# Optimization experiments

Hardware: AMD Instinct MI355X
Metric: run time of the kernel (lower is better)

Reference implementation:

```python
import jax, jax.numpy as jnp
import numpy as np

N = 100000   # nodes
E = 1600000  # edges (avg degree 16)
DIN, DH, DOUT = 128, 64, 40


def setup_inputs() -> dict:
    key = jax.random.key(0)
    ks = jax.random.split(key, 6)
    x = jax.random.normal(ks[0], (N, DIN), dtype=jnp.float32)
    edge_index = jax.random.randint(ks[1], (2, E), 0, N, dtype=jnp.int32)
    s1 = float(1.0 / np.sqrt(DIN))
    s2 = float(1.0 / np.sqrt(DH))
    W1 = jax.random.uniform(ks[2], (DIN, DH), jnp.float32, -s1, s1)
    b1 = jax.random.uniform(ks[3], (DH,), jnp.float32, -s1, s1)
    W2 = jax.random.uniform(ks[4], (DH, DOUT), jnp.float32, -s2, s2)
    b2 = jax.random.uniform(ks[5], (DOUT,), jnp.float32, -s2, s2)
    return {"x": x, "W1": W1, "b1": b1, "W2": W2, "b2": b2, "edge_index": edge_index}


def _gcn_conv(x, W, b, src, dst):
    """PyG GCNConv: add self-loops, symmetric degree normalization, scatter-add."""
    n = x.shape[0]
    h = x @ W  # [N, F_out] — transform before propagation (PyG order)
    ones = jnp.ones(src.shape[0], dtype=h.dtype)
    deg = jax.ops.segment_sum(ones, dst, num_segments=n) + 1.0  # +1 for self-loop
    dinv = jax.lax.rsqrt(deg)  # deg >= 1, no zero guard needed
    norm = dinv[src] * dinv[dst]  # [E]
    agg = jax.ops.segment_sum(h[src] * norm[:, None], dst, num_segments=n)
    agg = agg + h * (dinv * dinv)[:, None]  # self-loop messages
    return agg + b


def reference(x, W1, b1, W2, b2, edge_index):
    src, dst = edge_index[0], edge_index[1]
    h = jax.nn.relu(_gcn_conv(x, W1, b1, src, dst))
    out = _gcn_conv(h, W2, b2, src, dst)
    return jax.nn.log_softmax(out, axis=1)
```

## Files before the change

kernel.cpp:

```cpp
#include <hip/hip_runtime.h>
#include <hip/hip_fp16.h>
#include <math.h>

#define N_NODES 100000
#define N_EDGES 1600000
#define DIN 128
#define DH 64
#define DOUT 40

#define NB 256
#define BN 391
#define CAP 8192
#define BIN_BLOCKS 256
#define EPB 6250

typedef unsigned short u16;
typedef unsigned int u32;

__device__ inline __half2 u2h(u32 u) {
    union { u32 x; __half2 h; } c; c.x = u; return c.h;
}
__device__ inline u32 h2u(__half2 h) {
    union { __half2 h; u32 x; } c; c.h = h; return c.x;
}


__global__ __launch_bounds__(256) void k_bin(const int* __restrict__ src,
                                             const int* __restrict__ dst,
                                             int* __restrict__ gcur,
                                             u32* __restrict__ staged) {
    __shared__ int hist[NB];
    __shared__ int base[NB];
    __shared__ int cur[NB];
    int t = threadIdx.x;
    for (int i = t; i < NB; i += 256) { hist[i] = 0; cur[i] = 0; }
    __syncthreads();
    int e0 = blockIdx.x * EPB;
    int e1 = e0 + EPB; if (e1 > N_EDGES) e1 = N_EDGES;
    for (int e = e0 + t; e < e1; e += 256)
        atomicAdd(&hist[dst[e] / BN], 1);
    __syncthreads();
    for (int i = t; i < NB; i += 256) {
        int h = hist[i];
        base[i] = h ? atomicAdd(&gcur[i], h) : 0;
    }
    __syncthreads();
    for (int e = e0 + t; e < e1; e += 256) {
        int d = dst[e], s = src[e];
        int b = d / BN;
        int dl = d - b * BN;
        int r = base[b] + atomicAdd(&cur[b], 1);
        if (r < CAP) staged[(size_t)b * CAP + r] = (u32)s | ((u32)dl << 17);
    }
}


__global__ __launch_bounds__(256) void k_csr(const int* __restrict__ gcur,
                                             const u32* __restrict__ staged,
                                             int* __restrict__ csr,
                                             int4* __restrict__ meta,
                                             float* __restrict__ dinv) {
    __shared__ u32 sedge[CAP];
    __shared__ int lcsr[CAP];
    __shared__ int hist[BN];
    __shared__ int lrs[BN];
    __shared__ int cur[BN];
    __shared__ int sbuf[256];
    int b = blockIdx.x, t = threadIdx.x;

    int part = 0;
    for (int i = t; i < b; i += 256) {
        int c = gcur[i]; if (c > CAP) c = CAP;
        part += c;
    }
    sbuf[t] = part;
    __syncthreads();
    for (int off = 128; off; off >>= 1) {
        if (t < off) sbuf[t] += sbuf[t + off];
        __syncthreads();
    }
    int base_ = sbuf[0];
    __syncthreads();

    int cnt = gcur[b]; if (cnt > CAP) cnt = CAP;
    for (int i = t; i < BN; i += 256) hist[i] = 0;
    for (int i = t; i < cnt; i += 256) sedge[i] = staged[(size_t)b * CAP + i];
    __syncthreads();
    for (int i = t; i < cnt; i += 256) atomicAdd(&hist[sedge[i] >> 17], 1);
    __syncthreads();

    int v0 = (2 * t < BN) ? hist[2 * t] : 0;
    int v1 = (2 * t + 1 < BN) ? hist[2 * t + 1] : 0;
    int s = v0 + v1;
    sbuf[t] = s;
    __syncthreads();
    for (int off = 1; off < 256; off <<= 1) {
        int add = (t >= off) ? sbuf[t - off] : 0;
        __syncthreads();
        sbuf[t] += add;
        __syncthreads();
    }
    int excl = sbuf[t] - s;
    if (2 * t < BN)     { lrs[2 * t] = excl;      cur[2 * t] = excl; }
    if (2 * t + 1 < BN) { lrs[2 * t + 1] = excl + v0; cur[2 * t + 1] = excl + v0; }
    __syncthreads();

    for (int i = t; i < cnt; i += 256) {
        u32 p = sedge[i];
        int pos = atomicAdd(&cur[p >> 17], 1);
        lcsr[pos] = (int)((p & 0x1FFFF) << 3);
    }
    __syncthreads();

    for (int i = t; i < cnt; i += 256) csr[base_ + i] = lcsr[i];
    int n0 = b * BN;
    for (int i = t; i < BN; i += 256) {
        int n = n0 + i;
        if (n < N_NODES) {
            int dg = hist[i];
            float dv = rsqrtf((float)dg + 1.0f);
            meta[n] = make_int4(base_ + lrs[i], dg, __float_as_int(dv), 0);
            dinv[n] = dv;
        }
    }
}


__global__ __launch_bounds__(256) void k_gemm1(const float* __restrict__ x,
                                               const float* __restrict__ W1,
                                               const float* __restrict__ dinv,
                                               u16* __restrict__ h1s) {
    __shared__ float xs[64 * 140];
    __shared__ float wsh[DIN * DH];
    int t = threadIdx.x;
    int row0 = blockIdx.x * 64;

    for (int it = 0; it < 8; ++it) {
        int idx = (it * 256 + t) * 4;
        int r = idx >> 7, c = idx & 127;
        float4 v = make_float4(0.f, 0.f, 0.f, 0.f);
        if (row0 + r < N_NODES) v = *(const float4*)&x[(size_t)(row0 + r) * DIN + c];
        *(float4*)&xs[r * 140 + c] = v;
    }
    for (int it = 0; it < 8; ++it) {
        int idx = (it * 256 + t) * 4;
        *(float4*)&wsh[idx] = *(const float4*)&W1[idx];
    }
    __syncthreads();

    int tr = t & 15;
    int tc = t >> 4;
    float acc[4][4] = {};
    for (int kb = 0; kb < DIN; kb += 4) {
        float4 w0 = *(const float4*)&wsh[(kb + 0) * DH + tr * 4];
        float4 w1 = *(const float4*)&wsh[(kb + 1) * DH + tr * 4];
        float4 w2 = *(const float4*)&wsh[(kb + 2) * DH + tr * 4];
        float4 w3 = *(const float4*)&wsh[(kb + 3) * DH + tr * 4];
#pragma unroll
        for (int i = 0; i < 4; ++i) {
            float4 xv = *(const float4*)&xs[(tc * 4 + i) * 140 + kb];
            acc[i][0] += xv.x * w0.x; acc[i][1] += xv.x * w0.y;
            acc[i][2] += xv.x * w0.z; acc[i][3] += xv.x * w0.w;
            acc[i][0] += xv.y * w1.x; acc[i][1] += xv.y * w1.y;
            acc[i][2] += xv.y * w1.z; acc[i][3] += xv.y * w1.w;
            acc[i][0] += xv.z * w2.x; acc[i][1] += xv.z * w2.y;
            acc[i][2] += xv.z * w2.z; acc[i][3] += xv.z * w2.w;
            acc[i][0] += xv.w * w3.x; acc[i][1] += xv.w * w3.y;
            acc[i][2] += xv.w * w3.z; acc[i][3] += xv.w * w3.w;
        }
    }
#pragma unroll
    for (int i = 0; i < 4; ++i) {
        int row = row0 + tc * 4 + i;
        if (row < N_NODES) {
            float dv = dinv[row];
            ushort4 o;
            o.x = __half_as_ushort(__float2half(acc[i][0] * dv));
            o.y = __half_as_ushort(__float2half(acc[i][1] * dv));
            o.z = __half_as_ushort(__float2half(acc[i][2] * dv));
            o.w = __half_as_ushort(__float2half(acc[i][3] * dv));
            *(ushort4*)&h1s[(size_t)row * DH + tr * 4] = o;
        }
    }
}


__global__ __launch_bounds__(256) void k_agg1(const u16* __restrict__ h1s,
                                              const int4* __restrict__ meta,
                                              const int* __restrict__ csr,
                                              const float* __restrict__ b1,
                                              float* __restrict__ h1) {
    int node = blockIdx.x * 4 + (threadIdx.x >> 6);
    if (node >= N_NODES) return;
    node = __builtin_amdgcn_readfirstlane(node);
    int lane = threadIdx.x & 63;
    int es = lane >> 3, fq = lane & 7;
    int4 me = meta[node];
    int s0 = me.x, d = me.y;
    float dv = __int_as_float(me.z);
    const uint4* rows = (const uint4*)h1s;
    __half2 A0 = __float2half2_rn(0.f), A1 = A0, A2 = A0, A3 = A0;
    if (es == 0) {
        uint4 v = rows[(u32)(node * 8 + fq)];
        A0 = u2h(v.x); A1 = u2h(v.y); A2 = u2h(v.z); A3 = u2h(v.w);
    }
    for (int base = 0; base < d; base += 64) {
        int nn = d - base; if (nn > 64) nn = 64;
        int myidx = (lane < nn) ? csr[s0 + base + lane] : 0;
        int j = 0;
        for (; j + 16 <= nn; j += 16) {
            int x0 = __builtin_amdgcn_ds_bpermute((j + es) * 4, myidx);
            int x1 = __builtin_amdgcn_ds_bpermute((j + 8 + es) * 4, myidx);
            uint4 v0 = rows[(u32)(x0 + fq)];
            uint4 v1 = rows[(u32)(x1 + fq)];
            A0 = __hadd2(A0, u2h(v0.x)); A1 = __hadd2(A1, u2h(v0.y));
            A2 = __hadd2(A2, u2h(v0.z)); A3 = __hadd2(A3, u2h(v0.w));
            A0 = __hadd2(A0, u2h(v1.x)); A1 = __hadd2(A1, u2h(v1.y));
            A2 = __hadd2(A2, u2h(v1.z)); A3 = __hadd2(A3, u2h(v1.w));
        }
        for (; j < nn; j += 8) {
            int x = __builtin_amdgcn_ds_bpermute((j + es) * 4, myidx);
            if (j + es < nn) {
                uint4 v = rows[(u32)(x + fq)];
                A0 = __hadd2(A0, u2h(v.x)); A1 = __hadd2(A1, u2h(v.y));
                A2 = __hadd2(A2, u2h(v.z)); A3 = __hadd2(A3, u2h(v.w));
            }
        }
    }
#pragma unroll
    for (int off = 8; off <= 32; off <<= 1) {
        A0 = __hadd2(A0, u2h((u32)__shfl_xor((int)h2u(A0), off, 64)));
        A1 = __hadd2(A1, u2h((u32)__shfl_xor((int)h2u(A1), off, 64)));
        A2 = __hadd2(A2, u2h((u32)__shfl_xor((int)h2u(A2), off, 64)));
        A3 = __hadd2(A3, u2h((u32)__shfl_xor((int)h2u(A3), off, 64)));
    }
    if (es == 0) {
        float4 bva = ((const float4*)b1)[fq * 2 + 0];
        float4 bvb = ((const float4*)b1)[fq * 2 + 1];
        float4 oa, ob;
        oa.x = fmaxf(__low2float(A0)  * dv + bva.x, 0.f);
        oa.y = fmaxf(__high2float(A0) * dv + bva.y, 0.f);
        oa.z = fmaxf(__low2float(A1)  * dv + bva.z, 0.f);
        oa.w = fmaxf(__high2float(A1) * dv + bva.w, 0.f);
        ob.x = fmaxf(__low2float(A2)  * dv + bvb.x, 0.f);
        ob.y = fmaxf(__high2float(A2) * dv + bvb.y, 0.f);
        ob.z = fmaxf(__low2float(A3)  * dv + bvb.z, 0.f);
        ob.w = fmaxf(__high2float(A3) * dv + bvb.w, 0.f);
        ((float4*)h1)[(u32)(node * 16 + fq * 2 + 0)] = oa;
        ((float4*)h1)[(u32)(node * 16 + fq * 2 + 1)] = ob;
    }
}


__global__ __launch_bounds__(256) void k_gemm2(const float* __restrict__ h1,
                                               const float* __restrict__ W2,
                                               const float* __restrict__ dinv,
                                               u16* __restrict__ h2s) {
    __shared__ float xs[64 * 68];
    __shared__ float wsh[DH * DOUT];
    int t = threadIdx.x;
    int row0 = blockIdx.x * 64;

    for (int it = 0; it < 4; ++it) {
        int idx = (it * 256 + t) * 4;
        int r = idx >> 6, c = idx & 63;
        float4 v = make_float4(0.f, 0.f, 0.f, 0.f);
        if (row0 + r < N_NODES) v = *(const float4*)&h1[(size_t)(row0 + r) * DH + c];
        *(float4*)&xs[r * 68 + c] = v;
    }
    for (int idx = t * 4; idx < DH * DOUT; idx += 1024) {
        *(float4*)&wsh[idx] = *(const float4*)&W2[idx];
    }
    __syncthreads();

    int fg = t & 7;
    int rg = t >> 3;
    float acc[2][5] = {};
    for (int k = 0; k < DH; ++k) {
        float x0 = xs[(rg * 2 + 0) * 68 + k];
        float x1 = xs[(rg * 2 + 1) * 68 + k];
#pragma unroll
        for (int j = 0; j < 5; ++j) {
            float w = wsh[k * DOUT + fg * 5 + j];
            acc[0][j] += x0 * w;
            acc[1][j] += x1 * w;
        }
    }
#pragma unroll
    for (int i = 0; i < 2; ++i) {
        int row = row0 + rg * 2 + i;
        if (row < N_NODES) {
            float dvv = dinv[row];
#pragma unroll
            for (int j = 0; j < 5; ++j)
                h2s[(size_t)row * 64 + fg * 5 + j] =
                    __half_as_ushort(__float2half(acc[i][j] * dvv));
        }
    }
}


__global__ __launch_bounds__(256) void k_agg2(const u16* __restrict__ h2s,
                                              const int4* __restrict__ meta,
                                              const int* __restrict__ csr,
                                              const float* __restrict__ b2,
                                              float* __restrict__ out) {
    int node = blockIdx.x * 4 + (threadIdx.x >> 6);
    if (node >= N_NODES) return;
    node = __builtin_amdgcn_readfirstlane(node);
    int lane = threadIdx.x & 63;
    int es = lane >> 3, fq = lane & 7;
    bool act = fq < 5;
    int4 me = meta[node];
    int s0 = me.x, d = me.y;
    float dv = __int_as_float(me.z);
    const uint4* rows = (const uint4*)h2s;
    __half2 A0 = __float2half2_rn(0.f), A1 = A0, A2 = A0, A3 = A0;
    if (es == 0 && act) {
        uint4 v = rows[(u32)(node * 8 + fq)];
        A0 = u2h(v.x); A1 = u2h(v.y); A2 = u2h(v.z); A3 = u2h(v.w);
    }
    for (int base = 0; base < d; base += 64) {
        int nn = d - base; if (nn > 64) nn = 64;
        int myidx = (lane < nn) ? csr[s0 + base + lane] : 0;
        int j = 0;
        for (; j + 16 <= nn; j += 16) {
            int x0 = __builtin_amdgcn_ds_bpermute((j + es) * 4, myidx);
            int x1 = __builtin_amdgcn_ds_bpermute((j + 8 + es) * 4, myidx);
            if (act) {
                uint4 v0 = rows[(u32)(x0 + fq)];
                uint4 v1 = rows[(u32)(x1 + fq)];
                A0 = __hadd2(A0, u2h(v0.x)); A1 = __hadd2(A1, u2h(v0.y));
                A2 = __hadd2(A2, u2h(v0.z)); A3 = __hadd2(A3, u2h(v0.w));
                A0 = __hadd2(A0, u2h(v1.x)); A1 = __hadd2(A1, u2h(v1.y));
                A2 = __hadd2(A2, u2h(v1.z)); A3 = __hadd2(A3, u2h(v1.w));
            }
        }
        for (; j < nn; j += 8) {
            int x = __builtin_amdgcn_ds_bpermute((j + es) * 4, myidx);
            if (act && j + es < nn) {
                uint4 v = rows[(u32)(x + fq)];
                A0 = __hadd2(A0, u2h(v.x)); A1 = __hadd2(A1, u2h(v.y));
                A2 = __hadd2(A2, u2h(v.z)); A3 = __hadd2(A3, u2h(v.w));
            }
        }
    }
#pragma unroll
    for (int off = 8; off <= 32; off <<= 1) {
        A0 = __hadd2(A0, u2h((u32)__shfl_xor((int)h2u(A0), off, 64)));
        A1 = __hadd2(A1, u2h((u32)__shfl_xor((int)h2u(A1), off, 64)));
        A2 = __hadd2(A2, u2h((u32)__shfl_xor((int)h2u(A2), off, 64)));
        A3 = __hadd2(A3, u2h((u32)__shfl_xor((int)h2u(A3), off, 64)));
    }

    float4 bva = act ? ((const float4*)b2)[fq * 2 + 0] : make_float4(0.f, 0.f, 0.f, 0.f);
    float4 bvb = act ? ((const float4*)b2)[fq * 2 + 1] : make_float4(0.f, 0.f, 0.f, 0.f);
    float v0 = act ? __low2float(A0)  * dv + bva.x : -INFINITY;
    float v1 = act ? __high2float(A0) * dv + bva.y : -INFINITY;
    float v2 = act ? __low2float(A1)  * dv + bva.z : -INFINITY;
    float v3 = act ? __high2float(A1) * dv + bva.w : -INFINITY;
    float v4 = act ? __low2float(A2)  * dv + bvb.x : -INFINITY;
    float v5 = act ? __high2float(A2) * dv + bvb.y : -INFINITY;
    float v6 = act ? __low2float(A3)  * dv + bvb.z : -INFINITY;
    float v7 = act ? __high2float(A3) * dv + bvb.w : -INFINITY;
    float m = fmaxf(fmaxf(fmaxf(v0, v1), fmaxf(v2, v3)),
                    fmaxf(fmaxf(v4, v5), fmaxf(v6, v7)));
    m = fmaxf(m, __shfl_xor(m, 1, 64));
    m = fmaxf(m, __shfl_xor(m, 2, 64));
    m = fmaxf(m, __shfl_xor(m, 4, 64));
    float ex = 0.f;
    if (act) {
        ex = __expf(v0 - m) + __expf(v1 - m) + __expf(v2 - m) + __expf(v3 - m)
           + __expf(v4 - m) + __expf(v5 - m) + __expf(v6 - m) + __expf(v7 - m);
    }
    ex += __shfl_xor(ex, 1, 64);
    ex += __shfl_xor(ex, 2, 64);
    ex += __shfl_xor(ex, 4, 64);
    float lse = m + __logf(ex);
    if (es == 0 && act) {
        float4 oa = make_float4(v0 - lse, v1 - lse, v2 - lse, v3 - lse);
        float4 ob = make_float4(v4 - lse, v5 - lse, v6 - lse, v7 - lse);
        *(float4*)&out[(u32)(node * 40 + fq * 8 + 0)] = oa;
        *(float4*)&out[(u32)(node * 40 + fq * 8 + 4)] = ob;
    }
}


extern "C" void kernel_launch(void* const* d_in, const int* in_sizes, int n_in,
                              void* d_out, int out_size, void* d_ws, size_t ws_size,
                              hipStream_t stream) {
    const float* x  = (const float*)d_in[0];
    const float* W1 = (const float*)d_in[1];
    const float* b1 = (const float*)d_in[2];
    const float* W2 = (const float*)d_in[3];
    const float* b2 = (const float*)d_in[4];
    const int* eidx = (const int*)d_in[5];
    const int* srcp = eidx;
    const int* dstp = eidx + N_EDGES;
    float* out = (float*)d_out;

    char* w = (char*)d_ws;
    int* gcur    = (int*)w;   w += sizeof(int) * NB;
    float* dinv  = (float*)w; w += sizeof(float) * N_NODES + 48;
    int4* meta   = (int4*)w;  w += sizeof(int4) * N_NODES;
    u32* staged  = (u32*)w;   w += sizeof(u32) * (size_t)NB * CAP;
    int* csr     = (int*)w;   w += sizeof(int) * N_EDGES;
    u16* h1s     = (u16*)w;   w += sizeof(u16) * (size_t)N_NODES * DH;
    float* h1    = (float*)w; w += sizeof(float) * (size_t)N_NODES * DH;
    u16* h2s     = h1s;

    hipMemsetAsync(gcur, 0, sizeof(int) * NB, stream);
    k_bin<<<BIN_BLOCKS, 256, 0, stream>>>(srcp, dstp, gcur, staged);
    k_csr<<<NB, 256, 0, stream>>>(gcur, staged, csr, meta, dinv);
    k_gemm1<<<(N_NODES + 63) / 64, 256, 0, stream>>>(x, W1, dinv, h1s);
    k_agg1<<<(N_NODES + 3) / 4, 256, 0, stream>>>(h1s, meta, csr, b1, h1);
    k_gemm2<<<(N_NODES + 63) / 64, 256, 0, stream>>>(h1, W2, dinv, h2s);
    k_agg2<<<(N_NODES + 3) / 4, 256, 0, stream>>>(h2s, meta, csr, b2, out);
}
```

Baseline: 213.3 us.

## Merge CSR build and first GEMM into one launch; add nontemporal stores

Computes per-node degree with global atomics during binning, so the first GEMM no longer needs dinv from the CSR kernel. This lets CSR construction and GEMM1 run as disjoint block ranges of a single kernel, overlapping the two and removing one launch. Streaming loads and stores are also marked nontemporal to reduce cache pollution. The cost is 1.6M extra global atomics in the bin kernel, a larger memset, and higher shared-memory use per block, which may lower occupancy for the GEMM blocks.

After: 280.2 us. 1.31x slower.

```diff
diff --git a/kernel.cpp b/kernel.cpp
--- a/kernel.cpp
+++ b/kernel.cpp
@@ -13,21 +13,29 @@
 #define CAP 8192
 #define BIN_BLOCKS 256
 #define EPB 6250
+#define GEMM1_BLOCKS ((N_NODES + 63) / 64)
 
 typedef unsigned short u16;
 typedef unsigned int u32;
+typedef float f32x4 __attribute__((ext_vector_type(4)));
+typedef unsigned short u16x4 __attribute__((ext_vector_type(4)));
 
 __device__ inline __half2 u2h(u32 u) {
     union { u32 x; __half2 h; } c; c.x = u; return c.h;
 }
 __device__ inline u32 h2u(__half2 h) {
     union { __half2 h; u32 x; } c; c.h = h; return c.x;
+}
+__device__ inline void nt_store4(float* p, float a, float b, float c, float d) {
+    f32x4 t = {a, b, c, d};
+    __builtin_nontemporal_store(t, (f32x4*)p);
 }
 
 
 __global__ __launch_bounds__(256) void k_bin(const int* __restrict__ src,
                                              const int* __restrict__ dst,
                                              int* __restrict__ gcur,
+                                             int* __restrict__ deg,
                                              u32* __restrict__ staged) {
     __shared__ int hist[NB];
     __shared__ int base[NB];
@@ -37,8 +45,11 @@
     __syncthreads();
     int e0 = blockIdx.x * EPB;
     int e1 = e0 + EPB; if (e1 > N_EDGES) e1 = N_EDGES;
-    for (int e = e0 + t; e < e1; e += 256)
-        atomicAdd(&hist[dst[e] / BN], 1);
+    for (int e = e0 + t; e < e1; e += 256) {
+        int dd = dst[e];
+        atomicAdd(&hist[dd / BN], 1);
+        atomicAdd(&deg[dd], 1);
+    }
     __syncthreads();
     for (int i = t; i < NB; i += 256) {
         int h = hist[i];
@@ -50,136 +61,143 @@
         int b = d / BN;
         int dl = d - b * BN;
         int r = base[b] + atomicAdd(&cur[b], 1);
-        if (r < CAP) staged[(size_t)b * CAP + r] = (u32)s | ((u32)dl << 17);
-    }
-}
-
-
-__global__ __launch_bounds__(256) void k_csr(const int* __restrict__ gcur,
+        if (r < CAP)
+            __builtin_nontemporal_store((u32)s | ((u32)dl << 17),
+                                        &staged[(size_t)b * CAP + r]);
+    }
+}
+
+
+__global__ __launch_bounds__(256) void k_mid(const int* __restrict__ gcur,
                                              const u32* __restrict__ staged,
                                              int* __restrict__ csr,
                                              int4* __restrict__ meta,
-                                             float* __restrict__ dinv) {
-    __shared__ u32 sedge[CAP];
-    __shared__ int lcsr[CAP];
-    __shared__ int hist[BN];
-    __shared__ int lrs[BN];
-    __shared__ int cur[BN];
-    __shared__ int sbuf[256];
-    int b = blockIdx.x, t = threadIdx.x;
-
-    int part = 0;
-    for (int i = t; i < b; i += 256) {
-        int c = gcur[i]; if (c > CAP) c = CAP;
-        part += c;
-    }
-    sbuf[t] = part;
-    __syncthreads();
-    for (int off = 128; off; off >>= 1) {
-        if (t < off) sbuf[t] += sbuf[t + off];
-        __syncthreads();
-    }
-    int base_ = sbuf[0];
-    __syncthreads();
-
-    int cnt = gcur[b]; if (cnt > CAP) cnt = CAP;
-    for (int i = t; i < BN; i += 256) hist[i] = 0;
-    for (int i = t; i < cnt; i += 256) sedge[i] = staged[(size_t)b * CAP + i];
-    __syncthreads();
-    for (int i = t; i < cnt; i += 256) atomicAdd(&hist[sedge[i] >> 17], 1);
-    __syncthreads();
-
-    int v0 = (2 * t < BN) ? hist[2 * t] : 0;
-    int v1 = (2 * t + 1 < BN) ? hist[2 * t + 1] : 0;
-    int s = v0 + v1;
-    sbuf[t] = s;
-    __syncthreads();
-    for (int off = 1; off < 256; off <<= 1) {
-        int add = (t >= off) ? sbuf[t - off] : 0;
-        __syncthreads();
-        sbuf[t] += add;
-        __syncthreads();
-    }
-    int excl = sbuf[t] - s;
-    if (2 * t < BN)     { lrs[2 * t] = excl;      cur[2 * t] = excl; }
-    if (2 * t + 1 < BN) { lrs[2 * t + 1] = excl + v0; cur[2 * t + 1] = excl + v0; }
-    __syncthreads();
-
-    for (int i = t; i < cnt; i += 256) {
-        u32 p = sedge[i];
-        int pos = atomicAdd(&cur[p >> 17], 1);
-        lcsr[pos] = (int)((p & 0x1FFFF) << 3);
-    }
-    __syncthreads();
-
-    for (int i = t; i < cnt; i += 256) csr[base_ + i] = lcsr[i];
-    int n0 = b * BN;
-    for (int i = t; i < BN; i += 256) {
-        int n = n0 + i;
-        if (n < N_NODES) {
-            int dg = hist[i];
-            float dv = rsqrtf((float)dg + 1.0f);
-            meta[n] = make_int4(base_ + lrs[i], dg, __float_as_int(dv), 0);
-            dinv[n] = dv;
-        }
-    }
-}
-
-
-__global__ __launch_bounds__(256) void k_gemm1(const float* __restrict__ x,
-                                               const float* __restrict__ W1,
-                                               const float* __restrict__ dinv,
-                                               u16* __restrict__ h1s) {
-    __shared__ float xs[64 * 140];
-    __shared__ float wsh[DIN * DH];
+                                             float* __restrict__ dinv,
+                                             const int* __restrict__ deg,
+                                             const float* __restrict__ x,
+                                             const float* __restrict__ W1,
+                                             u16* __restrict__ h1s) {
+    __shared__ __align__(16) char smem[71296];
     int t = threadIdx.x;
-    int row0 = blockIdx.x * 64;
-
-    for (int it = 0; it < 8; ++it) {
-        int idx = (it * 256 + t) * 4;
-        int r = idx >> 7, c = idx & 127;
-        float4 v = make_float4(0.f, 0.f, 0.f, 0.f);
-        if (row0 + r < N_NODES) v = *(const float4*)&x[(size_t)(row0 + r) * DIN + c];
-        *(float4*)&xs[r * 140 + c] = v;
-    }
-    for (int it = 0; it < 8; ++it) {
-        int idx = (it * 256 + t) * 4;
-        *(float4*)&wsh[idx] = *(const float4*)&W1[idx];
-    }
-    __syncthreads();
-
-    int tr = t & 15;
-    int tc = t >> 4;
-    float acc[4][4] = {};
-    for (int kb = 0; kb < DIN; kb += 4) {
-        float4 w0 = *(const float4*)&wsh[(kb + 0) * DH + tr * 4];
-        float4 w1 = *(const float4*)&wsh[(kb + 1) * DH + tr * 4];
-        float4 w2 = *(const float4*)&wsh[(kb + 2) * DH + tr * 4];
-        float4 w3 = *(const float4*)&wsh[(kb + 3) * DH + tr * 4];
+    int blk = blockIdx.x;
+
+    if (blk < NB) {
+        u32* sedge = (u32*)smem;
+        int* lcsr  = (int*)(smem + 32768);
+        int* hist  = (int*)(smem + 65536);
+        int* lrs   = (int*)(smem + 67100);
+        int* cur   = (int*)(smem + 68664);
+        int* sbuf  = (int*)(smem + 70228);
+        int b = blk;
+
+        int part = 0;
+        for (int i = t; i < b; i += 256) {
+            int c = gcur[i]; if (c > CAP) c = CAP;
+            part += c;
+        }
+        sbuf[t] = part;
+        __syncthreads();
+        for (int off = 128; off; off >>= 1) {
+            if (t < off) sbuf[t] += sbuf[t + off];
+            __syncthreads();
+        }
+        int base_ = sbuf[0];
+        __syncthreads();
+
+        int cnt = gcur[b]; if (cnt > CAP) cnt = CAP;
+        for (int i = t; i < BN; i += 256) hist[i] = 0;
+        for (int i = t; i < cnt; i += 256)
+            sedge[i] = __builtin_nontemporal_load(&staged[(size_t)b * CAP + i]);
+        __syncthreads();
+        for (int i = t; i < cnt; i += 256) atomicAdd(&hist[sedge[i] >> 17], 1);
+        __syncthreads();
+
+        int v0 = (2 * t < BN) ? hist[2 * t] : 0;
+        int v1 = (2 * t + 1 < BN) ? hist[2 * t + 1] : 0;
+        int s = v0 + v1;
+        sbuf[t] = s;
+        __syncthreads();
+        for (int off = 1; off < 256; off <<= 1) {
+            int add = (t >= off) ? sbuf[t - off] : 0;
+            __syncthreads();
+            sbuf[t] += add;
+            __syncthreads();
+        }
+        int excl = sbuf[t] - s;
+        if (2 * t < BN)     { lrs[2 * t] = excl;          cur[2 * t] = excl; }
+        if (2 * t + 1 < BN) { lrs[2 * t + 1] = excl + v0; cur[2 * t + 1] = excl + v0; }
+        __syncthreads();
+
+        for (int i = t; i < cnt; i += 256) {
+            u32 p = sedge[i];
+            int pos = atomicAdd(&cur[p >> 17], 1);
+            lcsr[pos] = (int)((p & 0x1FFFF) << 3);
+        }
+        __syncthreads();
+
+        for (int i = t; i < cnt; i += 256)
+            __builtin_nontemporal_store(lcsr[i], &csr[base_ + i]);
+        int n0 = b * BN;
+        for (int i = t; i < BN; i += 256) {
+            int n = n0 + i;
+            if (n < N_NODES) {
+                int dg = hist[i];
+                float dv = rsqrtf((float)dg + 1.0f);
+                meta[n] = make_int4(base_ + lrs[i], dg, __float_as_int(dv), 0);
+                dinv[n] = dv;
+            }
+        }
+    } else {
+        float* xs  = (float*)smem;
+        float* wsh = (float*)(smem + 35840);
+        int row0 = (blk - NB) * 64;
+
+        for (int it = 0; it < 8; ++it) {
+            int idx = (it * 256 + t) * 4;
+            int r = idx >> 7, c = idx & 127;
+            float4 v = make_float4(0.f, 0.f, 0.f, 0.f);
+            if (row0 + r < N_NODES) v = *(const float4*)&x[(size_t)(row0 + r) * DIN + c];
+            *(float4*)&xs[r * 140 + c] = v;
+        }
+        for (int it = 0; it < 8; ++it) {
+            int idx = (it * 256 + t) * 4;
+            *(float4*)&wsh[idx] = *(const float4*)&W1[idx];
+        }
+        __syncthreads();
+
+        int tr = t & 15;
+        int tc = t >> 4;
+        float acc[4][4] = {};
+        for (int kb = 0; kb < DIN; kb += 4) {
+            float4 w0 = *(const float4*)&wsh[(kb + 0) * DH + tr * 4];
+            float4 w1 = *(const float4*)&wsh[(kb + 1) * DH + tr * 4];
+            float4 w2 = *(const float4*)&wsh[(kb + 2) * DH + tr * 4];
+            float4 w3 = *(const float4*)&wsh[(kb + 3) * DH + tr * 4];
+#pragma unroll
+            for (int i = 0; i < 4; ++i) {
+                float4 xv = *(const float4*)&xs[(tc * 4 + i) * 140 + kb];
+                acc[i][0] += xv.x * w0.x; acc[i][1] += xv.x * w0.y;
+                acc[i][2] += xv.x * w0.z; acc[i][3] += xv.x * w0.w;
+                acc[i][0] += xv.y * w1.x; acc[i][1] += xv.y * w1.y;
+                acc[i][2] += xv.y * w1.z; acc[i][3] += xv.y * w1.w;
+                acc[i][0] += xv.z * w2.x; acc[i][1] += xv.z * w2.y;
+                acc[i][2] += xv.z * w2.z; acc[i][3] += xv.z * w2.w;
+                acc[i][0] += xv.w * w3.x; acc[i][1] += xv.w * w3.y;
+                acc[i][2] += xv.w * w3.z; acc[i][3] += xv.w * w3.w;
+            }
+        }
 #pragma unroll
         for (int i = 0; i < 4; ++i) {
-            float4 xv = *(const float4*)&xs[(tc * 4 + i) * 140 + kb];
-            acc[i][0] += xv.x * w0.x; acc[i][1] += xv.x * w0.y;
-            acc[i][2] += xv.x * w0.z; acc[i][3] += xv.x * w0.w;
-            acc[i][0] += xv.y * w1.x; acc[i][1] += xv.y * w1.y;
-            acc[i][2] += xv.y * w1.z; acc[i][3] += xv.y * w1.w;
-            acc[i][0] += xv.z * w2.x; acc[i][1] += xv.z * w2.y;
-            acc[i][2] += xv.z * w2.z; acc[i][3] += xv.z * w2.w;
-            acc[i][0] += xv.w * w3.x; acc[i][1] += xv.w * w3.y;
-            acc[i][2] += xv.w * w3.z; acc[i][3] += xv.w * w3.w;
-        }
-    }
-#pragma unroll
-    for (int i = 0; i < 4; ++i) {
-        int row = row0 + tc * 4 + i;
-        if (row < N_NODES) {
-            float dv = dinv[row];
-            ushort4 o;
-            o.x = __half_as_ushort(__float2half(acc[i][0] * dv));
-            o.y = __half_as_ushort(__float2half(acc[i][1] * dv));
-            o.z = __half_as_ushort(__float2half(acc[i][2] * dv));
-            o.w = __half_as_ushort(__float2half(acc[i][3] * dv));
-            *(ushort4*)&h1s[(size_t)row * DH + tr * 4] = o;
+            int row = row0 + tc * 4 + i;
+            if (row < N_NODES) {
+                float dv = rsqrtf((float)deg[row] + 1.0f);
+                u16x4 o;
+                o.x = __half_as_ushort(__float2half(acc[i][0] * dv));
+                o.y = __half_as_ushort(__float2half(acc[i][1] * dv));
+                o.z = __half_as_ushort(__float2half(acc[i][2] * dv));
+                o.w = __half_as_ushort(__float2half(acc[i][3] * dv));
+                __builtin_nontemporal_store(o, (u16x4*)&h1s[(size_t)row * DH + tr * 4]);
+            }
         }
     }
 }
@@ -206,7 +224,7 @@
     }
     for (int base = 0; base < d; base += 64) {
         int nn = d - base; if (nn > 64) nn = 64;
-        int myidx = (lane < nn) ? csr[s0 + base + lane] : 0;
+        int myidx = (lane < nn) ? __builtin_nontemporal_load(&csr[s0 + base + lane]) : 0;
         int j = 0;
         for (; j + 16 <= nn; j += 16) {
             int x0 = __builtin_amdgcn_ds_bpermute((j + es) * 4, myidx);
@@ -237,17 +255,17 @@
     if (es == 0) {
         float4 bva = ((const float4*)b1)[fq * 2 + 0];
         float4 bvb = ((const float4*)b1)[fq * 2 + 1];
-        float4 oa, ob;
-        oa.x = fmaxf(__low2float(A0)  * dv + bva.x, 0.f);
-        oa.y = fmaxf(__high2float(A0) * dv + bva.y, 0.f);
-        oa.z = fmaxf(__low2float(A1)  * dv + bva.z, 0.f);
-        oa.w = fmaxf(__high2float(A1) * dv + bva.w, 0.f);
-        ob.x = fmaxf(__low2float(A2)  * dv + bvb.x, 0.f);
-        ob.y = fmaxf(__high2float(A2) * dv + bvb.y, 0.f);
-        ob.z = fmaxf(__low2float(A3)  * dv + bvb.z, 0.f);
-        ob.w = fmaxf(__high2float(A3) * dv + bvb.w, 0.f);
-        ((float4*)h1)[(u32)(node * 16 + fq * 2 + 0)] = oa;
-        ((float4*)h1)[(u32)(node * 16 + fq * 2 + 1)] = ob;
+        float* dst0 = &h1[(u32)(node * 64 + fq * 8)];
+        nt_store4(dst0,
+                  fmaxf(__low2float(A0)  * dv + bva.x, 0.f),
+                  fmaxf(__high2float(A0) * dv + bva.y, 0.f),
+                  fmaxf(__low2float(A1)  * dv + bva.z, 0.f),
+                  fmaxf(__high2float(A1) * dv + bva.w, 0.f));
+        nt_store4(dst0 + 4,
+                  fmaxf(__low2float(A2)  * dv + bvb.x, 0.f),
+                  fmaxf(__high2float(A2) * dv + bvb.y, 0.f),
+                  fmaxf(__low2float(A3)  * dv + bvb.z, 0.f),
+                  fmaxf(__high2float(A3) * dv + bvb.w, 0.f));
     }
 }
 
@@ -293,8 +311,9 @@
             float dvv = dinv[row];
 #pragma unroll
             for (int j = 0; j < 5; ++j)
-                h2s[(size_t)row * 64 + fg * 5 + j] =
-                    __half_as_ushort(__float2half(acc[i][j] * dvv));
+                __builtin_nontemporal_store(
+                    (u16)__half_as_ushort(__float2half(acc[i][j] * dvv)),
+                    &h2s[(size_t)row * 64 + fg * 5 + j]);
         }
     }
 }
@@ -322,7 +341,7 @@
     }
     for (int base = 0; base < d; base += 64) {
         int nn = d - base; if (nn > 64) nn = 64;
-        int myidx = (lane < nn) ? csr[s0 + base + lane] : 0;
+        int myidx = (lane < nn) ? __builtin_nontemporal_load(&csr[s0 + base + lane]) : 0;
         int j = 0;
         for (; j + 16 <= nn; j += 16) {
             int x0 = __builtin_amdgcn_ds_bpermute((j + es) * 4, myidx);
@@ -378,10 +397,9 @@
     ex += __shfl_xor(ex, 4, 64);
     float lse = m + __logf(ex);
     if (es == 0 && act) {
-        float4 oa = make_float4(v0 - lse, v1 - lse, v2 - lse, v3 - lse);
-        float4 ob = make_float4(v4 - lse, v5 - lse, v6 - lse, v7 - lse);
-        *(float4*)&out[(u32)(node * 40 + fq * 8 + 0)] = oa;
-        *(float4*)&out[(u32)(node * 40 + fq * 8 + 4)] = ob;
+        float* dst0 = &out[(u32)(node * 40 + fq * 8)];
+        nt_store4(dst0, v0 - lse, v1 - lse, v2 - lse, v3 - lse);
+        nt_store4(dst0 + 4, v4 - lse, v5 - lse, v6 - lse, v7 - lse);
     }
 }
 
@@ -401,7 +419,8 @@
 
     char* w = (char*)d_ws;
     int* gcur    = (int*)w;   w += sizeof(int) * NB;
-    float* dinv  = (float*)w; w += sizeof(float) * N_NODES + 48;
+    int* deg     = (int*)w;   w += sizeof(int) * N_NODES;
+    float* dinv  = (float*)w; w += sizeof(float) * N_NODES;
     int4* meta   = (int4*)w;  w += sizeof(int4) * N_NODES;
     u32* staged  = (u32*)w;   w += sizeof(u32) * (size_t)NB * CAP;
     int* csr     = (int*)w;   w += sizeof(int) * N_EDGES;
@@ -409,10 +428,10 @@
     float* h1    = (float*)w; w += sizeof(float) * (size_t)N_NODES * DH;
     u16* h2s     = h1s;
 
-    hipMemsetAsync(gcur, 0, sizeof(int) * NB, stream);
-    k_bin<<<BIN_BLOCKS, 256, 0, stream>>>(srcp, dstp, gcur, staged);
-    k_csr<<<NB, 256, 0, stream>>>(gcur, staged, csr, meta, dinv);
-    k_gemm1<<<(N_NODES + 63) / 64, 256, 0, stream>>>(x, W1, dinv, h1s);
+    hipMemsetAsync(gcur, 0, sizeof(int) * (NB + N_NODES), stream);
+    k_bin<<<BIN_BLOCKS, 256, 0, stream>>>(srcp, dstp, gcur, deg, staged);
+    k_mid<<<NB + GEMM1_BLOCKS, 256, 0, stream>>>(gcur, staged, csr, meta, dinv,
+                                                 deg, x, W1, h1s);
     k_agg1<<<(N_NODES + 3) / 4, 256, 0, stream>>>(h1s, meta, csr, b1, h1);
     k_gemm2<<<(N_NODES + 63) / 64, 256, 0, stream>>>(h1, W2, dinv, h2s);
     k_agg2<<<(N_NODES + 3) / 4, 256, 0, stream>>>(h2s, meta, csr, b2, out);
```
